# Kernel optimization log

Hardware: AMD Instinct MI355X
Metric: run time of the kernel (lower is better)

Reference implementation:

```python
import jax, jax.numpy as jnp
import numpy as np

N_MLPS = 256
N_BLOCKS = 8
TCODE = 13
IN_F = 3
HID = 128
OUT_F = 1
B = 256
NPTS = 2048
K = 256  # 8-bit codebook
OMEGA = 30.0

# per-layer (fan_in, fan_out) for weight reconstruction
LAYER_SHAPES = [(IN_F + TCODE, HID), (HID, HID), (HID, HID), (HID, OUT_F)]


def setup_inputs() -> dict:
    key = jax.random.key(0)
    ks = jax.random.split(key, 20)
    inp = {
        "x": jax.random.uniform(ks[0], (B, NPTS, IN_F), jnp.float32, -1.0, 1.0),
        "mlp_idx": jax.random.randint(ks[1], (B,), 0, N_MLPS, jnp.int32),
        "block_idx": jax.random.randint(ks[2], (B,), 0, N_BLOCKS, jnp.int32),
        "latent_table": jax.random.normal(ks[3], (N_MLPS, N_BLOCKS, TCODE), jnp.float32),
    }
    for l, (fi, fo) in enumerate(LAYER_SHAPES):
        bound = 1.0 / np.sqrt(fi)
        inp[f"centroids_l{l}"] = jax.random.uniform(ks[4 + 3 * l], (K,), jnp.float32, -bound, bound)
        inp[f"labels_l{l}"] = jax.random.randint(ks[5 + 3 * l], (N_MLPS * fi * fo,), 0, K, jnp.int32)
        inp[f"bias_l{l}"] = jax.random.uniform(ks[6 + 3 * l], (N_MLPS, 1, fo), jnp.float32, -bound, bound)
    return inp


def _layer(h, idx, centroids, labels, bias, fi, fo, apply_sin):
    # codebook dequant: weight.view(-1)[:] = centroids[labels]
    weight = centroids[labels].reshape(N_MLPS, fi, fo)
    # indexed bmm: torch.bmm(x, weight[indices]) + bias[indices]
    out = jnp.einsum("bni,bio->bno", h, weight[idx]) + bias[idx]
    return jnp.sin(OMEGA * out) if apply_sin else out


def reference(x, mlp_idx, block_idx, latent_table,
              centroids_l0, labels_l0, bias_l0,
              centroids_l1, labels_l1, bias_l1,
              centroids_l2, labels_l2, bias_l2,
              centroids_l3, labels_l3, bias_l3):
    # gather per-sample latent code and concat with coords
    z = latent_table[mlp_idx, block_idx]                      # [B, TCODE]
    h = jnp.concatenate(
        [x, jnp.broadcast_to(z[:, None, :], (x.shape[0], x.shape[1], TCODE))], axis=-1)
    cs = [centroids_l0, centroids_l1, centroids_l2, centroids_l3]
    ls = [labels_l0, labels_l1, labels_l2, labels_l3]
    bs = [bias_l0, bias_l1, bias_l2, bias_l3]
    for l, (fi, fo) in enumerate(LAYER_SHAPES):
        h = _layer(h, mlp_idx, cs[l], ls[l], bs[l], fi, fo, apply_sin=(l < len(LAYER_SHAPES) - 1))
    return h
```

## Files before the change

kernel.cpp:

```cpp
#include <hip/hip_runtime.h>


typedef unsigned int u32;
typedef unsigned short u16;
typedef __bf16 v8bf  __attribute__((ext_vector_type(8)));
typedef __bf16 v2bf  __attribute__((ext_vector_type(2)));
typedef float  v16f  __attribute__((ext_vector_type(16)));
typedef float  v2f   __attribute__((ext_vector_type(2)));
typedef u32    v4u   __attribute__((ext_vector_type(4)));
typedef u32    v2u   __attribute__((ext_vector_type(2)));

#define MFMA(a, b, c) __builtin_amdgcn_mfma_f32_32x32x16_bf16(a, b, c, 0, 0, 0)

#define HSTRIDE 136
#define OMEGA_S 4.774648292756860f

__device__ __forceinline__ float sinrev(float rev) {
    return __builtin_amdgcn_sinf(__builtin_amdgcn_fractf(rev));
}

__device__ __forceinline__ u32 pack2(float c) {
    __bf16 b0 = (__bf16)c;
    float  f0 = (float)b0;
    __bf16 b1 = (__bf16)(c - f0);
    return (u32)__builtin_bit_cast(u16, b0) |
           ((u32)__builtin_bit_cast(u16, b1) << 16);
}

__device__ __forceinline__ void pk2(float s0, float s1, u32& lo, u32& hi) {
    v2f s; s[0] = s0; s[1] = s1;
    v2bf l = __builtin_convertvector(s, v2bf);
    u32 lov = __builtin_bit_cast(u32, l);
    v2f lf;
    lf[0] = __builtin_bit_cast(float, lov << 16);
    lf[1] = __builtin_bit_cast(float, lov & 0xffff0000u);
    v2f r = s - lf;
    v2bf h = __builtin_convertvector(r, v2bf);
    lo = lov;
    hi = __builtin_bit_cast(u32, h);
}

__device__ __forceinline__ u32 pklo(float s0, float s1) {
    v2f s; s[0] = s0; s[1] = s1;
    v2bf l = __builtin_convertvector(s, v2bf);
    return __builtin_bit_cast(u32, l);
}

#define PLO(a, b) __builtin_amdgcn_perm((a), (b), 0x05040100u)
#define PHI(a, b) __builtin_amdgcn_perm((a), (b), 0x07060302u)

__global__ __launch_bounds__(512)
void ecnr_dequant(const float* __restrict__ cent0, const int* __restrict__ lab0,
                  const float* __restrict__ cent1, const int* __restrict__ lab1,
                  const float* __restrict__ cent2, const int* __restrict__ lab2,
                  const float* __restrict__ cent3, const int* __restrict__ lab3,
                  const float* __restrict__ bias0, const float* __restrict__ bias1,
                  const float* __restrict__ bias2,
                  u16* __restrict__ wpl1, u16* __restrict__ wpl2,
                  u16* __restrict__ w0pl, u16* __restrict__ w3pl,
                  float* __restrict__ biasc)
{
    __shared__ u32 cpk[512];
    const int t = threadIdx.x;

    if (blockIdx.x < 512) {
        const int m = blockIdx.x >> 1, L = blockIdx.x & 1;
        if (t < 256) cpk[t] = pack2((L ? cent2 : cent1)[t] * OMEGA_S);
        __syncthreads();
        const int* lab = (L ? lab2 : lab1) + (size_t)m * 16384;
        u16* base = (L ? wpl2 : wpl1) + (size_t)m * 32768;
        #pragma unroll
        for (int i = 0; i < 4; ++i) {
            const int id = i * 512 + t;
            const int n = id & 127, c = id >> 7;
            u32 g[8];
            #pragma unroll
            for (int j = 0; j < 8; ++j) g[j] = cpk[lab[(8 * c + j) * 128 + n]];
            v4u lo, hi;
            #pragma unroll
            for (int r = 0; r < 4; ++r) {
                lo[r] = PLO(g[2 * r + 1], g[2 * r]);
                hi[r] = PHI(g[2 * r + 1], g[2 * r]);
            }
            *(v4u*)(base + c * 1024 + n * 8)         = lo;
            *(v4u*)(base + 16384 + c * 1024 + n * 8) = hi;
        }
    } else {
        const int m = blockIdx.x - 512;
        if (t < 256) cpk[t] = pack2(cent0[t] * OMEGA_S);
        else         cpk[t] = pack2(cent3[t - 256]);
        __syncthreads();
        if (t < 256) {
            const int n = t & 127, c = t >> 7;
            const int* lab = lab0 + (size_t)m * 2048;
            u32 g[8];
            #pragma unroll
            for (int j = 0; j < 8; ++j) g[j] = cpk[lab[(8 * c + j) * 128 + n]];
            v4u lo, hi;
            #pragma unroll
            for (int r = 0; r < 4; ++r) {
                lo[r] = PLO(g[2 * r + 1], g[2 * r]);
                hi[r] = PHI(g[2 * r + 1], g[2 * r]);
            }
            u16* b0 = w0pl + (size_t)m * 4096;
            *(v4u*)(b0 + c * 1024 + n * 8)        = lo;
            *(v4u*)(b0 + 2048 + c * 1024 + n * 8) = hi;
        } else if (t < 384) {
            const int kk = t - 256;
            const u32 u = cpk[256 + lab3[(size_t)m * 128 + kk]];
            w3pl[(size_t)m * 256 + kk]       = (u16)u;
            w3pl[(size_t)m * 256 + 128 + kk] = (u16)(u >> 16);
        }
        if (t < 384) {
            const int li = t >> 7, kk = t & 127;
            const float* bsrc = (li == 0) ? bias0 : (li == 1) ? bias1 : bias2;
            biasc[(size_t)m * 384 + t] = bsrc[m * 128 + kk] * OMEGA_S;
        }
    }
}

__global__ __launch_bounds__(512, 8)
void ecnr_fwd(const float* __restrict__ x,
              const int*   __restrict__ mlp_idx,
              const int*   __restrict__ block_idx,
              const float* __restrict__ latent,
              const float* __restrict__ bias3,
              const u16* __restrict__ wpl1, const u16* __restrict__ wpl2,
              const u16* __restrict__ w0pl, const u16* __restrict__ w3pl,
              const float* __restrict__ biasc,
              float* __restrict__ out)
{
    __shared__ __attribute__((aligned(16))) u16   Hlo[64 * HSTRIDE];
    __shared__ __attribute__((aligned(16))) u16   Hhi[64 * HSTRIDE];
    __shared__ __attribute__((aligned(16))) float biasS[2 * 128];
    __shared__ __attribute__((aligned(16))) float red[2 * 128];

    const int g    = blockIdx.x;
    const int b    = ((g >> 8) << 3) | (g & 7);
    const int p0   = ((g >> 3) & 31) * 64;
    const int m    = mlp_idx[b];

    const int t  = threadIdx.x;
    const int l  = t & 63, w = t >> 6;
    const int q  = l >> 5, ln = l & 31;
    const int pt = w & 1, nt = w >> 1;
    const int mrow = pt * 32 + ln;
    const int nn   = nt * 32 + ln;
    const int bidx = nt * 32 + 4 * q;

    const float* bc = biasc + (size_t)m * 384;
    if (t < 128) {
        biasS[t]       = bc[128 + t];
        biasS[128 + t] = bc[256 + t];
    }
    const float* xp = x + (size_t)(b * 2048 + p0 + mrow) * 3;
    const float xv0 = xp[0], xv1 = xp[1], xv2 = xp[2];
    const u16* w0p = w0pl + (size_t)m * 4096 + q * 1024 + nn * 8;
    const v4u w0lo = *(const v4u*)(w0p);
    const v4u w0hi = *(const v4u*)(w0p + 2048);
    float4 b0f[4];
    #pragma unroll
    for (int gg = 0; gg < 4; ++gg)
        b0f[gg] = *(const float4*)(bc + bidx + 8 * gg);
    const float* zp = latent + ((size_t)m * 8 + block_idx[b]) * 13;
    float zr[8];
    #pragma unroll
    for (int j = 0; j < 8; ++j) zr[j] = zp[q * 5 + j];

    u16* lop = Hlo + mrow * HSTRIDE + nt * 32 + 4 * q;
    u16* hip = Hhi + mrow * HSTRIDE + nt * 32 + 4 * q;

    {
        float fin[8];
        if (q == 0) {
            fin[0] = xv0; fin[1] = xv1; fin[2] = xv2;
            #pragma unroll
            for (int j = 0; j < 5; ++j) fin[3 + j] = zr[j];
        } else {
            #pragma unroll
            for (int j = 0; j < 8; ++j) fin[j] = zr[j];
        }
        v4u il, ih;
        #pragma unroll
        for (int r = 0; r < 4; ++r) {
            u32 plo, phi;
            pk2(fin[2 * r], fin[2 * r + 1], plo, phi);
            il[r] = plo; ih[r] = phi;
        }
        const v8bf inlo = __builtin_bit_cast(v8bf, il);
        const v8bf inhi = __builtin_bit_cast(v8bf, ih);
        const v8bf wl = __builtin_bit_cast(v8bf, w0lo);
        const v8bf wh = __builtin_bit_cast(v8bf, w0hi);
        v16f acc;
        #pragma unroll
        for (int gg = 0; gg < 4; ++gg) {
            acc[4 * gg] = b0f[gg].x; acc[4 * gg + 1] = b0f[gg].y;
            acc[4 * gg + 2] = b0f[gg].z; acc[4 * gg + 3] = b0f[gg].w;
        }
        acc = MFMA(wl, inlo, acc);
        acc = MFMA(wl, inhi, acc);
        acc = MFMA(wh, inlo, acc);
        #pragma unroll
        for (int gg = 0; gg < 4; ++gg) {
            const float s0 = sinrev(acc[4 * gg + 0]);
            const float s1 = sinrev(acc[4 * gg + 1]);
            const float s2 = sinrev(acc[4 * gg + 2]);
            const float s3 = sinrev(acc[4 * gg + 3]);
            u32 l0, h0, l1, h1;
            pk2(s0, s1, l0, h0);
            pk2(s2, s3, l1, h1);
            v2u lov, hiv;
            lov[0] = l0; lov[1] = l1;
            hiv[0] = h0; hiv[1] = h1;
            *(v2u*)(lop + 8 * gg) = lov;
            *(v2u*)(hip + 8 * gg) = hiv;
        }
    }
    __syncthreads();

    const u16* HLO = Hlo + mrow * HSTRIDE + q * 8;
    const u16* HHI = Hhi + mrow * HSTRIDE + q * 8;
    #pragma unroll 1
    for (int L = 0; L < 2; ++L) {
        const u16* Wb = (L ? wpl2 : wpl1) + (size_t)m * 32768 + q * 1024 + nn * 8;
        v16f acc;
        #pragma unroll
        for (int gg = 0; gg < 4; ++gg) {
            const float4 bv = *(const float4*)&biasS[L * 128 + bidx + 8 * gg];
            acc[4 * gg] = bv.x; acc[4 * gg + 1] = bv.y;
            acc[4 * gg + 2] = bv.z; acc[4 * gg + 3] = bv.w;
        }
        v4u wl8[8];
        #pragma unroll
        for (int kc = 0; kc < 8; ++kc)
            wl8[kc] = *(const v4u*)(Wb + kc * 2048);
        #pragma unroll
        for (int kc = 0; kc < 8; ++kc) {
            const v4u whv = *(const v4u*)(Wb + kc * 2048 + 16384);
            const v8bf hlo = *(const v8bf*)(HLO + kc * 16);
            const v8bf hhi = *(const v8bf*)(HHI + kc * 16);
            acc = MFMA(__builtin_bit_cast(v8bf, wl8[kc]), hlo, acc);
            acc = MFMA(__builtin_bit_cast(v8bf, wl8[kc]), hhi, acc);
            acc = MFMA(__builtin_bit_cast(v8bf, whv), hlo, acc);
        }
        __syncthreads();
        if (L == 0) {
            #pragma unroll
            for (int gg = 0; gg < 4; ++gg) {
                const float s0 = sinrev(acc[4 * gg + 0]);
                const float s1 = sinrev(acc[4 * gg + 1]);
                const float s2 = sinrev(acc[4 * gg + 2]);
                const float s3 = sinrev(acc[4 * gg + 3]);
                u32 l0, h0, l1, h1;
                pk2(s0, s1, l0, h0);
                pk2(s2, s3, l1, h1);
                v2u lov, hiv;
                lov[0] = l0; lov[1] = l1;
                hiv[0] = h0; hiv[1] = h1;
                *(v2u*)(lop + 8 * gg) = lov;
                *(v2u*)(hip + 8 * gg) = hiv;
            }
        } else {
            #pragma unroll
            for (int gg = 0; gg < 4; ++gg) {
                const float s0 = sinrev(acc[4 * gg + 0]);
                const float s1 = sinrev(acc[4 * gg + 1]);
                const float s2 = sinrev(acc[4 * gg + 2]);
                const float s3 = sinrev(acc[4 * gg + 3]);
                v2u lov;
                lov[0] = pklo(s0, s1);
                lov[1] = pklo(s2, s3);
                *(v2u*)(lop + 8 * gg) = lov;
            }
        }
        __syncthreads();
    }

    {
        const u16* w3b = w3pl + (size_t)m * 256 + nt * 32 + q * 8;
        const u16* h3l = Hlo + mrow * HSTRIDE + nt * 32 + q * 8;
        v16f a3;
        #pragma unroll
        for (int r = 0; r < 16; ++r) a3[r] = 0.0f;
        #pragma unroll
        for (int kc = 0; kc < 2; ++kc) {
            const v8bf wl = *(const v8bf*)(w3b + kc * 16);
            const v8bf wh = *(const v8bf*)(w3b + 128 + kc * 16);
            const v8bf hl = *(const v8bf*)(h3l + kc * 16);
            a3 = MFMA(wl, hl, a3);
            a3 = MFMA(wh, hl, a3);
        }
        if (q == 0) red[pt * 128 + nt * 32 + ln] = a3[0];
    }
    __syncthreads();

    if (t < 64) {
        const int rp = (t >> 5) * 128, rl = t & 31;
        const float o = bias3[m]
            + red[rp + rl] + red[rp + 32 + rl]
            + red[rp + 64 + rl] + red[rp + 96 + rl];
        out[(size_t)b * 2048 + p0 + t] = o;
    }
}

extern "C" void kernel_launch(void* const* d_in, const int* in_sizes, int n_in,
                              void* d_out, int out_size, void* d_ws, size_t ws_size,
                              hipStream_t stream) {
    (void)in_sizes; (void)n_in; (void)out_size; (void)ws_size;
    u16*   wpl1  = (u16*)d_ws;
    u16*   wpl2  = wpl1 + (size_t)256 * 32768;
    u16*   w0pl  = wpl2 + (size_t)256 * 32768;
    u16*   w3pl  = w0pl + (size_t)256 * 4096;
    float* biasc = (float*)(w3pl + (size_t)256 * 256);

    ecnr_dequant<<<768, 512, 0, stream>>>(
        (const float*)d_in[4],  (const int*)d_in[5],
        (const float*)d_in[7],  (const int*)d_in[8],
        (const float*)d_in[10], (const int*)d_in[11],
        (const float*)d_in[13], (const int*)d_in[14],
        (const float*)d_in[6],  (const float*)d_in[9], (const float*)d_in[12],
        wpl1, wpl2, w0pl, w3pl, biasc);

    ecnr_fwd<<<8192, 512, 0, stream>>>(
        (const float*)d_in[0], (const int*)d_in[1], (const int*)d_in[2],
        (const float*)d_in[3],
        (const float*)d_in[15],
        wpl1, wpl2, w0pl, w3pl, biasc,
        (float*)d_out);
}
```

Before: 236.8 us.

## Fuse final 128->1 layer into layer-2 epilogue as fp32 FMA dot product

The last layer's output (fan_out 1) is now computed directly from the layer-2 accumulators. Each lane multiplies sin(acc) by preloaded fp32 layer-3 weights and writes partial sums to shared memory, where eight partials per point are reduced. This drops the bf16 write of layer-2 activations, two barriers, and the padded MFMA pass for the output layer. In exchange each thread holds 16 more registers of weights, and the last layer now runs in full fp32 rather than split-bf16.

```diff
diff --git a/kernel.cpp b/kernel.cpp
--- a/kernel.cpp
+++ b/kernel.cpp
@@ -40,12 +40,6 @@
     hi = __builtin_bit_cast(u32, h);
 }
 
-__device__ __forceinline__ u32 pklo(float s0, float s1) {
-    v2f s; s[0] = s0; s[1] = s1;
-    v2bf l = __builtin_convertvector(s, v2bf);
-    return __builtin_bit_cast(u32, l);
-}
-
 #define PLO(a, b) __builtin_amdgcn_perm((a), (b), 0x05040100u)
 #define PHI(a, b) __builtin_amdgcn_perm((a), (b), 0x07060302u)
 
@@ -57,10 +51,10 @@
                   const float* __restrict__ bias0, const float* __restrict__ bias1,
                   const float* __restrict__ bias2,
                   u16* __restrict__ wpl1, u16* __restrict__ wpl2,
-                  u16* __restrict__ w0pl, u16* __restrict__ w3pl,
+                  u16* __restrict__ w0pl, float* __restrict__ w3f,
                   float* __restrict__ biasc)
 {
-    __shared__ u32 cpk[512];
+    __shared__ u32 cpk[256];
     const int t = threadIdx.x;
 
     if (blockIdx.x < 512) {
@@ -88,7 +82,6 @@
     } else {
         const int m = blockIdx.x - 512;
         if (t < 256) cpk[t] = pack2(cent0[t] * OMEGA_S);
-        else         cpk[t] = pack2(cent3[t - 256]);
         __syncthreads();
         if (t < 256) {
             const int n = t & 127, c = t >> 7;
@@ -107,9 +100,7 @@
             *(v4u*)(b0 + 2048 + c * 1024 + n * 8) = hi;
         } else if (t < 384) {
             const int kk = t - 256;
-            const u32 u = cpk[256 + lab3[(size_t)m * 128 + kk]];
-            w3pl[(size_t)m * 256 + kk]       = (u16)u;
-            w3pl[(size_t)m * 256 + 128 + kk] = (u16)(u >> 16);
+            w3f[(size_t)m * 128 + kk] = cent3[lab3[(size_t)m * 128 + kk]];
         }
         if (t < 384) {
             const int li = t >> 7, kk = t & 127;
@@ -126,14 +117,14 @@
               const float* __restrict__ latent,
               const float* __restrict__ bias3,
               const u16* __restrict__ wpl1, const u16* __restrict__ wpl2,
-              const u16* __restrict__ w0pl, const u16* __restrict__ w3pl,
+              const u16* __restrict__ w0pl, const float* __restrict__ w3f,
               const float* __restrict__ biasc,
               float* __restrict__ out)
 {
     __shared__ __attribute__((aligned(16))) u16   Hlo[64 * HSTRIDE];
     __shared__ __attribute__((aligned(16))) u16   Hhi[64 * HSTRIDE];
     __shared__ __attribute__((aligned(16))) float biasS[2 * 128];
-    __shared__ __attribute__((aligned(16))) float red[2 * 128];
+    __shared__ __attribute__((aligned(16))) float red[2 * 256];
 
     const int g    = blockIdx.x;
     const int b    = ((g >> 8) << 3) | (g & 7);
@@ -166,6 +157,13 @@
     float zr[8];
     #pragma unroll
     for (int j = 0; j < 8; ++j) zr[j] = zp[q * 5 + j];
+    float w3v[16];
+    {
+        const float* w3b = w3f + (size_t)m * 128;
+        #pragma unroll
+        for (int r = 0; r < 16; ++r)
+            w3v[r] = w3b[nt * 32 + (r & 3) + 8 * (r >> 2) + 4 * q];
+    }
 
     u16* lop = Hlo + mrow * HSTRIDE + nt * 32 + 4 * q;
     u16* hip = Hhi + mrow * HSTRIDE + nt * 32 + 4 * q;
@@ -243,8 +241,8 @@
             acc = MFMA(__builtin_bit_cast(v8bf, wl8[kc]), hhi, acc);
             acc = MFMA(__builtin_bit_cast(v8bf, whv), hlo, acc);
         }
-        __syncthreads();
         if (L == 0) {
+            __syncthreads();
             #pragma unroll
             for (int gg = 0; gg < 4; ++gg) {
                 const float s0 = sinrev(acc[4 * gg + 0]);
@@ -260,45 +258,22 @@
                 *(v2u*)(lop + 8 * gg) = lov;
                 *(v2u*)(hip + 8 * gg) = hiv;
             }
+            __syncthreads();
         } else {
-            #pragma unroll
-            for (int gg = 0; gg < 4; ++gg) {
-                const float s0 = sinrev(acc[4 * gg + 0]);
-                const float s1 = sinrev(acc[4 * gg + 1]);
-                const float s2 = sinrev(acc[4 * gg + 2]);
-                const float s3 = sinrev(acc[4 * gg + 3]);
-                v2u lov;
-                lov[0] = pklo(s0, s1);
-                lov[1] = pklo(s2, s3);
-                *(v2u*)(lop + 8 * gg) = lov;
-            }
-        }
-        __syncthreads();
-    }
-
-    {
-        const u16* w3b = w3pl + (size_t)m * 256 + nt * 32 + q * 8;
-        const u16* h3l = Hlo + mrow * HSTRIDE + nt * 32 + q * 8;
-        v16f a3;
-        #pragma unroll
-        for (int r = 0; r < 16; ++r) a3[r] = 0.0f;
-        #pragma unroll
-        for (int kc = 0; kc < 2; ++kc) {
-            const v8bf wl = *(const v8bf*)(w3b + kc * 16);
-            const v8bf wh = *(const v8bf*)(w3b + 128 + kc * 16);
-            const v8bf hl = *(const v8bf*)(h3l + kc * 16);
-            a3 = MFMA(wl, hl, a3);
-            a3 = MFMA(wh, hl, a3);
-        }
-        if (q == 0) red[pt * 128 + nt * 32 + ln] = a3[0];
+            float s = 0.0f;
+            #pragma unroll
+            for (int r = 0; r < 16; ++r)
+                s = __builtin_fmaf(w3v[r], sinrev(acc[r]), s);
+            red[pt * 256 + (nt * 2 + q) * 32 + ln] = s;
+        }
     }
     __syncthreads();
 
     if (t < 64) {
-        const int rp = (t >> 5) * 128, rl = t & 31;
-        const float o = bias3[m]
-            + red[rp + rl] + red[rp + 32 + rl]
-            + red[rp + 64 + rl] + red[rp + 96 + rl];
+        const float* rp = red + (t >> 5) * 256 + (t & 31);
+        float o = bias3[m];
+        #pragma unroll
+        for (int gg = 0; gg < 8; ++gg) o += rp[gg * 32];
         out[(size_t)b * 2048 + p0 + t] = o;
     }
 }
@@ -310,8 +285,8 @@
     u16*   wpl1  = (u16*)d_ws;
     u16*   wpl2  = wpl1 + (size_t)256 * 32768;
     u16*   w0pl  = wpl2 + (size_t)256 * 32768;
-    u16*   w3pl  = w0pl + (size_t)256 * 4096;
-    float* biasc = (float*)(w3pl + (size_t)256 * 256);
+    float* w3f   = (float*)(w0pl + (size_t)256 * 4096);
+    float* biasc = w3f + (size_t)256 * 128;
 
     ecnr_dequant<<<768, 512, 0, stream>>>(
         (const float*)d_in[4],  (const int*)d_in[5],
@@ -319,12 +294,12 @@
         (const float*)d_in[10], (const int*)d_in[11],
         (const float*)d_in[13], (const int*)d_in[14],
         (const float*)d_in[6],  (const float*)d_in[9], (const float*)d_in[12],
-        wpl1, wpl2, w0pl, w3pl, biasc);
+        wpl1, wpl2, w0pl, w3f, biasc);
 
     ecnr_fwd<<<8192, 512, 0, stream>>>(
         (const float*)d_in[0], (const int*)d_in[1], (const int*)d_in[2],
         (const float*)d_in[3],
         (const float*)d_in[15],
-        wpl1, wpl2, w0pl, w3pl, biasc,
+        wpl1, wpl2, w0pl, w3f, biasc,
         (float*)d_out);
 }
```

Measured after the change: 248.8 us. 1.05x slower.
